# Kernel tuning notes

Measured on AMD Instinct MI355X. Metric: run time of the kernel, lower is better.

Reference implementation:

```python
import jax, jax.numpy as jnp
import numpy as np

B, D, C = 8192, 2048, 1000

def setup_inputs() -> dict:
    key = jax.random.key(0)
    k1, k2, k3 = jax.random.split(key, 3)
    x = jax.random.normal(k1, (B, D), dtype=jnp.float32)
    W = jax.random.normal(k2, (D, C), dtype=jnp.float32) * (1.0 / np.sqrt(D))
    b = jax.random.normal(k3, (C,), dtype=jnp.float32) * 0.01
    return {"x": x, "W": W, "b": b}

def reference(x, W, b):
    # inner classifier: logits out[b, c]
    out = jnp.dot(x, W) + b  # [B, C]
    # leave-one-out logsumexp per class, fused:
    # lse_k = logsumexp(out[:, != k]) = lse_all + log1p(-exp(out_k - lse_all))
    lse = jax.nn.logsumexp(out, axis=1, keepdims=True)  # [B, 1]
    loo = lse + jnp.log1p(-jnp.exp(out - lse))           # [B, C]
    # c_out = -loo; return c_out + out
    return out - loo
```

## Files before the change

### kernel.cpp

```cpp
#include <hip/hip_runtime.h>
#include <hip/hip_bf16.h>
#include <math.h>

#define BDIM 8192
#define DDIM 2048
#define CDIM 1000
#define NPAD 1024
#define BK   64

typedef __attribute__((ext_vector_type(8))) short short8;
typedef __attribute__((ext_vector_type(4))) float floatx4;

__device__ __forceinline__ unsigned short f2bf(float f) {
    union { float f; unsigned u; } a; a.f = f;
    unsigned u = a.u;
    u = (u + 0x7fff + ((u >> 16) & 1)) >> 16;
    return (unsigned short)u;
}

__device__ __forceinline__ void async_copy16(const void* gp, void* lp) {
    __builtin_amdgcn_global_load_lds(
        (const __attribute__((address_space(1))) void*)gp,
        (__attribute__((address_space(3))) void*)lp,
        16, 0, 0);
}

__global__ __launch_bounds__(256) void cvt_x_kernel(
    const float4* __restrict__ x, ushort4* __restrict__ xb)
{
    int i = blockIdx.x * 256 + threadIdx.x;
    float4 v = x[i];
    ushort4 o;
    o.x = f2bf(v.x); o.y = f2bf(v.y); o.z = f2bf(v.z); o.w = f2bf(v.w);
    xb[i] = o;
}

__global__ __launch_bounds__(256) void cvt_w_kernel(
    const float* __restrict__ W, unsigned short* __restrict__ Bt)
{
    __shared__ float tile[32][33];
    int k0 = blockIdx.x * 32;
    int n0 = blockIdx.y * 32;
    int tx = threadIdx.x, ty = threadIdx.y;
    #pragma unroll
    for (int i = 0; i < 4; i++) {
        int k = k0 + ty + i * 8;
        int n = n0 + tx;
        tile[ty + i * 8][tx] = (n < CDIM) ? W[(size_t)k * CDIM + n] : 0.0f;
    }
    __syncthreads();
    #pragma unroll
    for (int i = 0; i < 4; i++) {
        int n = n0 + ty + i * 8;
        int k = k0 + tx;
        Bt[(size_t)n * DDIM + k] = f2bf(tile[tx][ty + i * 8]);
    }
}

__global__ __launch_bounds__(256, 2) void gemm_bt_kernel(
    const unsigned short* __restrict__ A,
    const unsigned short* __restrict__ Bt,
    float* __restrict__ C)
{
    __shared__ unsigned short As[128 * BK];
    __shared__ unsigned short Bs[128 * BK];

    const int t    = threadIdx.x;
    const int wave = t >> 6;
    const int lane = t & 63;
    const int wm   = wave & 1;
    const int wn   = wave >> 1;
    const int quad = lane >> 4;
    const int l16  = lane & 15;

    const int mBase = blockIdx.y * 128;
    const int nBase = blockIdx.x * 128;

    floatx4 acc[4][4] = {};

    const int byteoff = t * 16;
    const int rowA    = byteoff >> 7;
    const int colb    = byteoff & 127;
    const char* Ag = (const char*)A  + ((size_t)(mBase + rowA) * DDIM) * 2 + colb;
    const char* Bg = (const char*)Bt + ((size_t)(nBase + rowA) * DDIM) * 2 + colb;
    char* AsDst = (char*)As + byteoff;
    char* BsDst = (char*)Bs + byteoff;

    for (int kt = 0; kt < DDIM; kt += BK) {
        const char* a = Ag + kt * 2;
        const char* b = Bg + kt * 2;
        #pragma unroll
        for (int r = 0; r < 4; r++) {
            async_copy16(a + (size_t)r * 32 * DDIM * 2, AsDst + r * 4096);
            async_copy16(b + (size_t)r * 32 * DDIM * 2, BsDst + r * 4096);
        }
        __syncthreads();

        #pragma unroll
        for (int ks = 0; ks < 2; ks++) {
            short8 af[4], bfr[4];
            #pragma unroll
            for (int mi = 0; mi < 4; mi++)
                af[mi] = *(const short8*)(As + (wm * 64 + mi * 16 + l16) * BK + ks * 32 + quad * 8);
            #pragma unroll
            for (int ni = 0; ni < 4; ni++)
                bfr[ni] = *(const short8*)(Bs + (wn * 64 + ni * 16 + l16) * BK + ks * 32 + quad * 8);
            #pragma unroll
            for (int mi = 0; mi < 4; mi++)
                #pragma unroll
                for (int ni = 0; ni < 4; ni++)
                    acc[mi][ni] = __builtin_amdgcn_mfma_f32_16x16x32_bf16(
                        af[mi], bfr[ni], acc[mi][ni], 0, 0, 0);
        }
        __syncthreads();
    }

    #pragma unroll
    for (int mi = 0; mi < 4; mi++) {
        int row0 = mBase + wm * 64 + mi * 16 + quad * 4;
        #pragma unroll
        for (int ni = 0; ni < 4; ni++) {
            int col = nBase + wn * 64 + ni * 16 + l16;
            if (col < CDIM) {
                #pragma unroll
                for (int rg = 0; rg < 4; rg++)
                    C[(size_t)(row0 + rg) * CDIM + col] = acc[mi][ni][rg];
            }
        }
    }
}

__global__ __launch_bounds__(256) void lse_kernel(
    float* __restrict__ C, const float* __restrict__ bias)
{
    const int row = blockIdx.x;
    const int t   = threadIdx.x;
    __shared__ float red[8];

    const bool valid = t < (CDIM / 4);
    const int c0 = t * 4;

    float4 v = make_float4(-INFINITY, -INFINITY, -INFINITY, -INFINITY);
    if (valid) {
        v = *(const float4*)(C + (size_t)row * CDIM + c0);
        float4 bb = *(const float4*)(bias + c0);
        v.x += bb.x; v.y += bb.y; v.z += bb.z; v.w += bb.w;
    }

    float m = fmaxf(fmaxf(v.x, v.y), fmaxf(v.z, v.w));
    #pragma unroll
    for (int off = 32; off > 0; off >>= 1)
        m = fmaxf(m, __shfl_down(m, off, 64));
    const int wave = t >> 6;
    if ((t & 63) == 0) red[wave] = m;
    __syncthreads();
    if (t == 0) red[4] = fmaxf(fmaxf(red[0], red[1]), fmaxf(red[2], red[3]));
    __syncthreads();
    const float M = red[4];

    float4 e = make_float4(0.f, 0.f, 0.f, 0.f);
    float s = 0.f;
    if (valid) {
        e.x = expf(v.x - M); e.y = expf(v.y - M);
        e.z = expf(v.z - M); e.w = expf(v.w - M);
        s = e.x + e.y + e.z + e.w;
    }
    #pragma unroll
    for (int off = 32; off > 0; off >>= 1)
        s += __shfl_down(s, off, 64);
    if ((t & 63) == 0) red[wave] = s;
    __syncthreads();
    if (t == 0) red[4] = red[0] + red[1] + red[2] + red[3];
    __syncthreads();
    const float S   = red[4];
    const float lse = M + logf(S);
    const float invS = 1.0f / S;

    if (valid) {
        float4 o;
        o.x = (v.x - lse) - log1pf(-e.x * invS);
        o.y = (v.y - lse) - log1pf(-e.y * invS);
        o.z = (v.z - lse) - log1pf(-e.z * invS);
        o.w = (v.w - lse) - log1pf(-e.w * invS);
        *(float4*)(C + (size_t)row * CDIM + c0) = o;
    }
}

extern "C" void kernel_launch(void* const* d_in, const int* in_sizes, int n_in,
                              void* d_out, int out_size, void* d_ws, size_t ws_size,
                              hipStream_t stream) {
    const float* x = (const float*)d_in[0];
    const float* W = (const float*)d_in[1];
    const float* b = (const float*)d_in[2];
    float* out = (float*)d_out;

    unsigned short* xb = (unsigned short*)d_ws;
    unsigned short* Bt = xb + (size_t)BDIM * DDIM;

    cvt_x_kernel<<<16384, 256, 0, stream>>>((const float4*)x, (ushort4*)xb);

    dim3 gw(DDIM / 32, NPAD / 32), bw(32, 8);
    cvt_w_kernel<<<gw, bw, 0, stream>>>(W, Bt);

    dim3 gg(NPAD / 128, BDIM / 128);
    gemm_bt_kernel<<<gg, 256, 0, stream>>>(xb, Bt, out);

    lse_kernel<<<BDIM, 256, 0, stream>>>(out, b);
}
```

Measured before the change: 192.8 us.

## Split GEMM along K into two halves, fuse conversions, remap tiles per XCD

Merges the x and W bf16 conversion kernels into one launch. The GEMM is split along K into two halves when the workspace is large enough, doubling the block count from 512 to 1024 so more of the GPU is filled. The two fp32 partial results are summed inside the LSE kernel. Block-to-tile mapping is rearranged so neighbouring tiles land on the same XCD for L2 reuse. The cost is an extra 32MB partial buffer that is written and read back, plus a workspace-size-dependent code path.

```diff
diff --git a/kernel.cpp b/kernel.cpp
--- a/kernel.cpp
+++ b/kernel.cpp
@@ -8,6 +8,11 @@
 #define NPAD 1024
 #define BK   64
 
+#define WS_XB_BYTES   33554432ULL
+#define WS_BT_BYTES    4194304ULL
+#define WS_C1_OFFSET  37748736ULL
+#define WS_NEED       70516736ULL
+
 typedef __attribute__((ext_vector_type(8))) short short8;
 typedef __attribute__((ext_vector_type(4))) float floatx4;
 
@@ -25,46 +30,47 @@
         16, 0, 0);
 }
 
-__global__ __launch_bounds__(256) void cvt_x_kernel(
-    const float4* __restrict__ x, ushort4* __restrict__ xb)
-{
-    int i = blockIdx.x * 256 + threadIdx.x;
-    float4 v = x[i];
-    ushort4 o;
-    o.x = f2bf(v.x); o.y = f2bf(v.y); o.z = f2bf(v.z); o.w = f2bf(v.w);
-    xb[i] = o;
-}
-
-__global__ __launch_bounds__(256) void cvt_w_kernel(
+__global__ __launch_bounds__(256) void cvt_kernel(
+    const float* __restrict__ x, unsigned short* __restrict__ xb,
     const float* __restrict__ W, unsigned short* __restrict__ Bt)
 {
-    __shared__ float tile[32][33];
-    int k0 = blockIdx.x * 32;
-    int n0 = blockIdx.y * 32;
-    int tx = threadIdx.x, ty = threadIdx.y;
-    #pragma unroll
-    for (int i = 0; i < 4; i++) {
-        int k = k0 + ty + i * 8;
-        int n = n0 + tx;
-        tile[ty + i * 8][tx] = (n < CDIM) ? W[(size_t)k * CDIM + n] : 0.0f;
-    }
-    __syncthreads();
-    #pragma unroll
-    for (int i = 0; i < 4; i++) {
-        int n = n0 + ty + i * 8;
-        int k = k0 + tx;
-        Bt[(size_t)n * DDIM + k] = f2bf(tile[tx][ty + i * 8]);
-    }
-}
-
-__global__ __launch_bounds__(256, 2) void gemm_bt_kernel(
+    const int blk = blockIdx.x;
+    const int t   = threadIdx.x;
+    if (blk < 16384) {
+        int i = blk * 256 + t;
+        float4 v = ((const float4*)x)[i];
+        ushort4 o;
+        o.x = f2bf(v.x); o.y = f2bf(v.y); o.z = f2bf(v.z); o.w = f2bf(v.w);
+        ((ushort4*)xb)[i] = o;
+    } else {
+        __shared__ float tile[32][33];
+        const int b2 = blk - 16384;
+        const int k0 = (b2 & 63) * 32;
+        const int n0 = (b2 >> 6) * 32;
+        const int tx = t & 31, ty = t >> 5;
+        #pragma unroll
+        for (int i = 0; i < 4; i++) {
+            int k = k0 + ty + i * 8;
+            int n = n0 + tx;
+            tile[ty + i * 8][tx] = (n < CDIM) ? W[(size_t)k * CDIM + n] : 0.0f;
+        }
+        __syncthreads();
+        #pragma unroll
+        for (int i = 0; i < 4; i++) {
+            int n = n0 + ty + i * 8;
+            int k = k0 + tx;
+            Bt[(size_t)n * DDIM + k] = f2bf(tile[tx][ty + i * 8]);
+        }
+    }
+}
+
+__device__ __forceinline__ void gemm_body(
     const unsigned short* __restrict__ A,
     const unsigned short* __restrict__ Bt,
-    float* __restrict__ C)
-{
-    __shared__ unsigned short As[128 * BK];
-    __shared__ unsigned short Bs[128 * BK];
-
+    float* __restrict__ C,
+    int mBase, int nBase, int kBase, int kIters,
+    unsigned short* As, unsigned short* Bs)
+{
     const int t    = threadIdx.x;
     const int wave = t >> 6;
     const int lane = t & 63;
@@ -73,20 +79,17 @@
     const int quad = lane >> 4;
     const int l16  = lane & 15;
 
-    const int mBase = blockIdx.y * 128;
-    const int nBase = blockIdx.x * 128;
-
     floatx4 acc[4][4] = {};
 
     const int byteoff = t * 16;
     const int rowA    = byteoff >> 7;
     const int colb    = byteoff & 127;
-    const char* Ag = (const char*)A  + ((size_t)(mBase + rowA) * DDIM) * 2 + colb;
-    const char* Bg = (const char*)Bt + ((size_t)(nBase + rowA) * DDIM) * 2 + colb;
+    const char* Ag = (const char*)A  + ((size_t)(mBase + rowA) * DDIM + kBase) * 2 + colb;
+    const char* Bg = (const char*)Bt + ((size_t)(nBase + rowA) * DDIM + kBase) * 2 + colb;
     char* AsDst = (char*)As + byteoff;
     char* BsDst = (char*)Bs + byteoff;
 
-    for (int kt = 0; kt < DDIM; kt += BK) {
+    for (int kt = 0; kt < kIters * BK; kt += BK) {
         const char* a = Ag + kt * 2;
         const char* b = Bg + kt * 2;
         #pragma unroll
@@ -130,8 +133,46 @@
     }
 }
 
+__global__ __launch_bounds__(256, 4) void gemm_splitk_kernel(
+    const unsigned short* __restrict__ A,
+    const unsigned short* __restrict__ Bt,
+    float* __restrict__ C0, float* __restrict__ C1)
+{
+    __shared__ unsigned short As[128 * BK];
+    __shared__ unsigned short Bs[128 * BK];
+
+    const int L   = blockIdx.x;
+    const int xcd = L & 7;
+    const int s   = L >> 3;
+    const int mz  = xcd * 16 + (s >> 3);
+    const int n_t = s & 7;
+    const int m_t = mz >> 1;
+    const int z   = mz & 1;
+
+    float* C = z ? C1 : C0;
+    gemm_body(A, Bt, C, m_t * 128, n_t * 128, z * (DDIM / 2), (DDIM / 2) / BK, As, Bs);
+}
+
+__global__ __launch_bounds__(256, 2) void gemm_single_kernel(
+    const unsigned short* __restrict__ A,
+    const unsigned short* __restrict__ Bt,
+    float* __restrict__ C0)
+{
+    __shared__ unsigned short As[128 * BK];
+    __shared__ unsigned short Bs[128 * BK];
+
+    const int L   = blockIdx.x;
+    const int xcd = L & 7;
+    const int s   = L >> 3;
+    const int m_t = xcd * 8 + (s >> 3);
+    const int n_t = s & 7;
+
+    gemm_body(A, Bt, C0, m_t * 128, n_t * 128, 0, DDIM / BK, As, Bs);
+}
+
 __global__ __launch_bounds__(256) void lse_kernel(
-    float* __restrict__ C, const float* __restrict__ bias)
+    float* __restrict__ C, const float* C1,
+    const float* __restrict__ bias, int split)
 {
     const int row = blockIdx.x;
     const int t   = threadIdx.x;
@@ -143,6 +184,10 @@
     float4 v = make_float4(-INFINITY, -INFINITY, -INFINITY, -INFINITY);
     if (valid) {
         v = *(const float4*)(C + (size_t)row * CDIM + c0);
+        if (split) {
+            float4 p = *(const float4*)(C1 + (size_t)row * CDIM + c0);
+            v.x += p.x; v.y += p.y; v.z += p.z; v.w += p.w;
+        }
         float4 bb = *(const float4*)(bias + c0);
         v.x += bb.x; v.y += bb.y; v.z += bb.z; v.w += bb.w;
     }
@@ -172,8 +217,8 @@
     __syncthreads();
     if (t == 0) red[4] = red[0] + red[1] + red[2] + red[3];
     __syncthreads();
-    const float S   = red[4];
-    const float lse = M + logf(S);
+    const float S    = red[4];
+    const float lse  = M + logf(S);
     const float invS = 1.0f / S;
 
     if (valid) {
@@ -196,14 +241,16 @@
 
     unsigned short* xb = (unsigned short*)d_ws;
     unsigned short* Bt = xb + (size_t)BDIM * DDIM;
-
-    cvt_x_kernel<<<16384, 256, 0, stream>>>((const float4*)x, (ushort4*)xb);
-
-    dim3 gw(DDIM / 32, NPAD / 32), bw(32, 8);
-    cvt_w_kernel<<<gw, bw, 0, stream>>>(W, Bt);
-
-    dim3 gg(NPAD / 128, BDIM / 128);
-    gemm_bt_kernel<<<gg, 256, 0, stream>>>(xb, Bt, out);
-
-    lse_kernel<<<BDIM, 256, 0, stream>>>(out, b);
-}
+    float* C1 = (float*)((char*)d_ws + WS_C1_OFFSET);
+    const bool splitk = ws_size >= WS_NEED;
+
+    cvt_kernel<<<18432, 256, 0, stream>>>(x, xb, W, Bt);
+
+    if (splitk) {
+        gemm_splitk_kernel<<<1024, 256, 0, stream>>>(xb, Bt, out, C1);
+        lse_kernel<<<BDIM, 256, 0, stream>>>(out, C1, b, 1);
+    } else {
+        gemm_single_kernel<<<512, 256, 0, stream>>>(xb, Bt, out);
+        lse_kernel<<<BDIM, 256, 0, stream>>>(out, nullptr, b, 0);
+    }
+}
```

After: 184.2 us. 1.05x faster.
